# Kernel optimization log

Hardware: AMD Instinct MI355X
Metric: run time of the kernel (lower is better)

The kernel has to match this reference:

```python
import jax, jax.numpy as jnp
import numpy as np

N = 100000
E = 1600000
IN, HID, OUT = 128, 128, 64


def sage_conv(x, edge_index, W_l, W_r, b):
    # PyG SAGEConv with mean aggregation:
    # out = mean_{j in N(i)} x_j @ W_l + x_i @ W_r + b
    src, dst = edge_index[0], edge_index[1]
    msgs = x[src]                                            # [E, D] gather
    summed = jax.ops.segment_sum(msgs, dst, num_segments=N)  # [N, D] scatter-add
    deg = jax.ops.segment_sum(jnp.ones((E,), x.dtype), dst, num_segments=N)
    mean = summed / jnp.maximum(deg, 1.0)[:, None]
    return mean @ W_l + x @ W_r + b


def setup_inputs() -> dict:
    key = jax.random.key(0)
    ks = jax.random.split(key, 8)
    x = jax.random.normal(ks[0], (N, IN), dtype=jnp.float32)
    edge_index = jax.random.randint(ks[1], (2, E), 0, N, dtype=jnp.int64)
    s1 = 1.0 / np.sqrt(IN)
    s2 = 1.0 / np.sqrt(HID)
    W1_l = jax.random.uniform(ks[2], (IN, HID), jnp.float32, -s1, s1)
    W1_r = jax.random.uniform(ks[3], (IN, HID), jnp.float32, -s1, s1)
    b1 = jnp.zeros((HID,), jnp.float32)
    W2_l = jax.random.uniform(ks[4], (HID, OUT), jnp.float32, -s2, s2)
    W2_r = jax.random.uniform(ks[5], (HID, OUT), jnp.float32, -s2, s2)
    b2 = jnp.zeros((OUT,), jnp.float32)
    return {"x": x, "edge_index": edge_index, "W1_l": W1_l, "W1_r": W1_r,
            "b1": b1, "W2_l": W2_l, "W2_r": W2_r, "b2": b2}


def reference(x, edge_index, W1_l, W1_r, b1, W2_l, W2_r, b2):
    h = sage_conv(x, edge_index, W1_l, W1_r, b1)
    h = jax.nn.relu(h)
    out = sage_conv(h, edge_index, W2_l, W2_r, b2)
    return out
```

## Files before the change

kernel.cpp:

```cpp
#include <hip/hip_runtime.h>

#define NN 100000
#define NE 1600000
#define KB 782
#define BSH 7
#define MAXB 4096
#define PBLK 200

#define OFF_CC    0
#define OFF_RST   1024
#define OFF_RDG   101120
#define OFF_STAGE 201216
#define OFF_XB    3404288
#define OFF_XF8   9810432
#define OFF_MEANB 13013504
#define OFF_HB    19419648
#define OFF_W1LP  25825792
#define OFF_W1RP  (25825792 + 8192)
#define OFF_W2LP  (25825792 + 16384)
#define OFF_W2RP  (25825792 + 20480)

typedef __bf16 bf16x8 __attribute__((ext_vector_type(8)));
typedef float f32x4 __attribute__((ext_vector_type(4)));
typedef float f32x2 __attribute__((ext_vector_type(2)));

static __device__ __forceinline__ ushort f2bf(float f) {
    unsigned u = __float_as_uint(f);
    return (ushort)((u + 0x7fffu + ((u >> 16) & 1u)) >> 16);
}
static __device__ __forceinline__ float bflo(unsigned u) { return __uint_as_float(u << 16); }
static __device__ __forceinline__ float bfhi(unsigned u) { return __uint_as_float(u & 0xffff0000u); }

__global__ void cvt_kernel(const float* __restrict__ x, ushort* __restrict__ xb,
                           unsigned* __restrict__ xf8) {
    int i = blockIdx.x * 256 + threadIdx.x;
    float4 v = ((const float4*)x)[i];
    uint2 o;
    o.x = (unsigned)f2bf(v.x) | ((unsigned)f2bf(v.y) << 16);
    o.y = (unsigned)f2bf(v.z) | ((unsigned)f2bf(v.w) << 16);
    ((uint2*)xb)[i] = o;
    int p8 = __builtin_amdgcn_cvt_pk_fp8_f32(v.x, v.y, 0, false);
    p8 = __builtin_amdgcn_cvt_pk_fp8_f32(v.z, v.w, p8, true);
    xf8[i] = (unsigned)p8;
}

__global__ void pack_kernel(const float* __restrict__ W1l, const float* __restrict__ W1r,
                            const float* __restrict__ W2l, const float* __restrict__ W2r,
                            ushort* __restrict__ w1lp, ushort* __restrict__ w1rp,
                            ushort* __restrict__ w2lp, ushort* __restrict__ w2rp) {
    int blk = blockIdx.x;
    const float* W;
    ushort* out;
    int N, frag0;
    if (blk < 8)       { W = W1l; out = w1lp; N = 128; frag0 = blk * 4; }
    else if (blk < 16) { W = W1r; out = w1rp; N = 128; frag0 = (blk - 8) * 4; }
    else if (blk < 20) { W = W2l; out = w2lp; N = 64;  frag0 = (blk - 16) * 4; }
    else               { W = W2r; out = w2rp; N = 64;  frag0 = (blk - 20) * 4; }
    int lane = threadIdx.x & 63;
    int frag = frag0 + (threadIdx.x >> 6);
    int NT = N >> 4;
    int ktile = frag / NT, ntile = frag - ktile * NT;
    int k = ktile * 32 + (lane >> 4) * 8;
    int n = ntile * 16 + (lane & 15);
    ushort tmp[8];
#pragma unroll
    for (int j = 0; j < 8; ++j) tmp[j] = f2bf(W[(k + j) * N + n]);
    uint4 o;
    o.x = (unsigned)tmp[0] | ((unsigned)tmp[1] << 16);
    o.y = (unsigned)tmp[2] | ((unsigned)tmp[3] << 16);
    o.z = (unsigned)tmp[4] | ((unsigned)tmp[5] << 16);
    o.w = (unsigned)tmp[6] | ((unsigned)tmp[7] << 16);
    *(uint4*)&out[(frag * 64 + lane) * 8] = o;
}

__global__ __launch_bounds__(1024) void cpart_kernel(const int* __restrict__ src,
                                                     const int* __restrict__ dst,
                                                     int* __restrict__ cc,
                                                     unsigned* __restrict__ stage) {
    __shared__ int hist[KB];
    __shared__ int cur[KB];
    int t = threadIdx.x;
    int e0 = blockIdx.x * (NE / PBLK);
    int e1 = e0 + (NE / PBLK);
    for (int i = t; i < KB; i += 1024) hist[i] = 0;
    __syncthreads();
    for (int e = e0 + t; e < e1; e += 1024)
        atomicAdd(&hist[dst[e] >> BSH], 1);
    __syncthreads();
    for (int i = t; i < KB; i += 1024) {
        int c = hist[i];
        cur[i] = c ? atomicAdd(&cc[i], c) : 0;
    }
    __syncthreads();
    for (int e = e0 + t; e < e1; e += 1024) {
        int d = dst[e];
        int bkt = d >> BSH;
        int p = atomicAdd(&cur[bkt], 1);
        if (p < MAXB)
            stage[bkt * MAXB + p] = ((unsigned)(d & 127) << 17) | (unsigned)src[e];
    }
}

__global__ __launch_bounds__(256) void sort_kernel(unsigned* __restrict__ stage,
                                                   const int* __restrict__ cc,
                                                   int* __restrict__ rstart,
                                                   int* __restrict__ rdeg) {
    __shared__ unsigned ssrc[MAXB];
    __shared__ int sc[128];
    __shared__ int loff[129];
    __shared__ int lcur[128];
    int t = threadIdx.x;
    int b = blockIdx.x;
    unsigned* st = stage + b * MAXB;
    int cnt = min(cc[b], MAXB);

    if (t < 128) lcur[t] = 0;
    __syncthreads();
    for (int i = t; i < cnt; i += 256) atomicAdd(&lcur[st[i] >> 17], 1);
    __syncthreads();
    if (t < 128) sc[t] = lcur[t];
    __syncthreads();
    for (int off = 1; off < 128; off <<= 1) {
        int v = (t < 128 && t >= off) ? sc[t - off] : 0;
        __syncthreads();
        if (t < 128) sc[t] += v;
        __syncthreads();
    }
    if (t < 128) {
        int excl = (t == 0) ? 0 : sc[t - 1];
        loff[t] = excl;
        lcur[t] = excl;
    }
    if (t == 127) loff[128] = sc[127];
    __syncthreads();
    for (int i = t; i < cnt; i += 256) {
        unsigned v = st[i];
        int p = atomicAdd(&lcur[v >> 17], 1);
        ssrc[p] = v & 0x1FFFFu;
    }
    __syncthreads();
    for (int i = t; i < cnt; i += 256) st[i] = ssrc[i];
    int node0 = b << BSH;
    if (t < 128 && node0 + t < NN) {
        rstart[node0 + t] = b * MAXB + loff[t];
        rdeg[node0 + t] = loff[t + 1] - loff[t];
    }
}

__global__ __launch_bounds__(256) void agg1g_kernel(const unsigned* __restrict__ es,
                                                    const int* __restrict__ rstart,
                                                    const int* __restrict__ rdeg,
                                                    const unsigned* __restrict__ xf8,
                                                    ushort* __restrict__ meanb) {
    int t = threadIdx.x;
    int node = blockIdx.x * 16 + (t >> 4);
    int l4 = t & 15;
    int s0 = rstart[node];
    int deg = rdeg[node];
    const uint2* xv = (const uint2*)xf8;
    float a0 = 0.f, a1 = 0.f, a2 = 0.f, a3 = 0.f;
    float a4 = 0.f, a5 = 0.f, a6 = 0.f, a7 = 0.f;
    int e = 0;
    for (; e + 4 <= deg; e += 4) {
        int q0 = es[s0 + e + 0];
        int q1 = es[s0 + e + 1];
        int q2 = es[s0 + e + 2];
        int q3 = es[s0 + e + 3];
        uint2 u0 = xv[q0 * 16 + l4];
        uint2 u1 = xv[q1 * 16 + l4];
        uint2 u2 = xv[q2 * 16 + l4];
        uint2 u3 = xv[q3 * 16 + l4];
#pragma unroll
        for (int j = 0; j < 4; ++j) {
            unsigned lo = (j == 0) ? u0.x : (j == 1) ? u1.x : (j == 2) ? u2.x : u3.x;
            unsigned hi = (j == 0) ? u0.y : (j == 1) ? u1.y : (j == 2) ? u2.y : u3.y;
            f32x2 p0 = __builtin_amdgcn_cvt_pk_f32_fp8(lo, false);
            f32x2 p1 = __builtin_amdgcn_cvt_pk_f32_fp8(lo, true);
            f32x2 p2 = __builtin_amdgcn_cvt_pk_f32_fp8(hi, false);
            f32x2 p3 = __builtin_amdgcn_cvt_pk_f32_fp8(hi, true);
            a0 += p0.x; a1 += p0.y; a2 += p1.x; a3 += p1.y;
            a4 += p2.x; a5 += p2.y; a6 += p3.x; a7 += p3.y;
        }
    }
    for (; e < deg; ++e) {
        uint2 u = xv[es[s0 + e] * 16 + l4];
        f32x2 p0 = __builtin_amdgcn_cvt_pk_f32_fp8(u.x, false);
        f32x2 p1 = __builtin_amdgcn_cvt_pk_f32_fp8(u.x, true);
        f32x2 p2 = __builtin_amdgcn_cvt_pk_f32_fp8(u.y, false);
        f32x2 p3 = __builtin_amdgcn_cvt_pk_f32_fp8(u.y, true);
        a0 += p0.x; a1 += p0.y; a2 += p1.x; a3 += p1.y;
        a4 += p2.x; a5 += p2.y; a6 += p3.x; a7 += p3.y;
    }
    float inv = 1.0f / fmaxf((float)deg, 1.0f);
    uint4 o;
    o.x = (unsigned)f2bf(a0 * inv) | ((unsigned)f2bf(a1 * inv) << 16);
    o.y = (unsigned)f2bf(a2 * inv) | ((unsigned)f2bf(a3 * inv) << 16);
    o.z = (unsigned)f2bf(a4 * inv) | ((unsigned)f2bf(a5 * inv) << 16);
    o.w = (unsigned)f2bf(a6 * inv) | ((unsigned)f2bf(a7 * inv) << 16);
    *(uint4*)&meanb[node * 128 + 8 * l4] = o;
}

__global__ __launch_bounds__(256) void agg2g_kernel(const unsigned* __restrict__ es,
                                                    const int* __restrict__ rstart,
                                                    const int* __restrict__ rdeg,
                                                    const ushort* __restrict__ pb,
                                                    float* __restrict__ meanp) {
    int t = threadIdx.x;
    int node = blockIdx.x * 8 + (t >> 5);
    int l5 = t & 31;
    int s0 = rstart[node];
    int deg = rdeg[node];
    const unsigned* pbu = (const unsigned*)pb;
    float a0 = 0.f, a1 = 0.f;
    int e = 0;
    for (; e + 4 <= deg; e += 4) {
        unsigned u0 = pbu[es[s0 + e + 0] * 32 + l5];
        unsigned u1 = pbu[es[s0 + e + 1] * 32 + l5];
        unsigned u2 = pbu[es[s0 + e + 2] * 32 + l5];
        unsigned u3 = pbu[es[s0 + e + 3] * 32 + l5];
        a0 += bflo(u0) + bflo(u1) + bflo(u2) + bflo(u3);
        a1 += bfhi(u0) + bfhi(u1) + bfhi(u2) + bfhi(u3);
    }
    for (; e < deg; ++e) {
        unsigned u = pbu[es[s0 + e] * 32 + l5];
        a0 += bflo(u); a1 += bfhi(u);
    }
    float inv = 1.0f / fmaxf((float)deg, 1.0f);
    float2 o = {a0 * inv, a1 * inv};
    *(float2*)&meanp[node * 64 + 2 * l5] = o;
}

__global__ __launch_bounds__(256) void gemm1_kernel(const ushort* __restrict__ meanb,
                                                    const ushort* __restrict__ xb,
                                                    const ushort* __restrict__ w1lp,
                                                    const ushort* __restrict__ w1rp,
                                                    const float* __restrict__ b1,
                                                    const ushort* __restrict__ w2lp,
                                                    ushort* __restrict__ hb,
                                                    ushort* __restrict__ pb) {
    __shared__ ushort As[64 * 136];
    int t = threadIdx.x;
    int node0 = blockIdx.x * 64;
    int w = t >> 6, l = t & 63;
    int lrow = w * 16 + (l & 15);
    int lkq = (l >> 4) * 8;
    int cq = l & 15, rq = (l >> 4) * 4;

    f32x4 acc[8];
#pragma unroll
    for (int i = 0; i < 8; ++i) acc[i] = (f32x4){0.f, 0.f, 0.f, 0.f};

    {
        const uint4* g = (const uint4*)(meanb + (size_t)node0 * 128);
#pragma unroll
        for (int i = 0; i < 4; ++i) {
            int chunk = t + 256 * i;
            *(uint4*)&As[(chunk >> 4) * 136 + (chunk & 15) * 8] = g[chunk];
        }
    }
    __syncthreads();
#pragma unroll
    for (int kt = 0; kt < 4; ++kt) {
        bf16x8 a = *(const bf16x8*)&As[lrow * 136 + kt * 32 + lkq];
        const bf16x8* bp = (const bf16x8*)w1lp + (kt * 8) * 64 + l;
#pragma unroll
        for (int nt = 0; nt < 8; ++nt)
            acc[nt] = __builtin_amdgcn_mfma_f32_16x16x32_bf16(a, bp[nt * 64], acc[nt], 0, 0, 0);
    }
    __syncthreads();

    {
        const uint4* g = (const uint4*)(xb + (size_t)node0 * 128);
#pragma unroll
        for (int i = 0; i < 4; ++i) {
            int chunk = t + 256 * i;
            *(uint4*)&As[(chunk >> 4) * 136 + (chunk & 15) * 8] = g[chunk];
        }
    }
    __syncthreads();
#pragma unroll
    for (int kt = 0; kt < 4; ++kt) {
        bf16x8 a = *(const bf16x8*)&As[lrow * 136 + kt * 32 + lkq];
        const bf16x8* bp = (const bf16x8*)w1rp + (kt * 8) * 64 + l;
#pragma unroll
        for (int nt = 0; nt < 8; ++nt)
            acc[nt] = __builtin_amdgcn_mfma_f32_16x16x32_bf16(a, bp[nt * 64], acc[nt], 0, 0, 0);
    }
    __syncthreads();

#pragma unroll
    for (int nt = 0; nt < 8; ++nt) {
        int n = nt * 16 + cq;
        float bias = b1[n];
#pragma unroll
        for (int r = 0; r < 4; ++r) {
            float hv = fmaxf(acc[nt][r] + bias, 0.0f);
            As[(w * 16 + rq + r) * 136 + n] = f2bf(hv);
        }
    }
    __syncthreads();

    {
        uint4* g = (uint4*)(hb + (size_t)node0 * 128);
#pragma unroll
        for (int i = 0; i < 4; ++i) {
            int chunk = t + 256 * i;
            if (node0 + (chunk >> 4) < NN)
                g[chunk] = *(const uint4*)&As[(chunk >> 4) * 136 + (chunk & 15) * 8];
        }
    }

    f32x4 acc2[4];
#pragma unroll
    for (int i = 0; i < 4; ++i) acc2[i] = (f32x4){0.f, 0.f, 0.f, 0.f};
#pragma unroll
    for (int kt = 0; kt < 4; ++kt) {
        bf16x8 a = *(const bf16x8*)&As[lrow * 136 + kt * 32 + lkq];
        const bf16x8* bp = (const bf16x8*)w2lp + (kt * 4) * 64 + l;
#pragma unroll
        for (int nt = 0; nt < 4; ++nt)
            acc2[nt] = __builtin_amdgcn_mfma_f32_16x16x32_bf16(a, bp[nt * 64], acc2[nt], 0, 0, 0);
    }
    __syncthreads();

#pragma unroll
    for (int nt = 0; nt < 4; ++nt)
#pragma unroll
        for (int r = 0; r < 4; ++r)
            As[(w * 16 + rq + r) * 136 + nt * 16 + cq] = f2bf(acc2[nt][r]);
    __syncthreads();
    {
        uint4* g = (uint4*)(pb + (size_t)node0 * 64);
#pragma unroll
        for (int i = 0; i < 2; ++i) {
            int chunk = t + 256 * i;
            if (node0 + (chunk >> 3) < NN)
                g[chunk] = *(const uint4*)&As[(chunk >> 3) * 136 + (chunk & 7) * 8];
        }
    }
}

__global__ __launch_bounds__(256) void gemm2_kernel(const float* __restrict__ meanp,
                                                    const ushort* __restrict__ hb,
                                                    const ushort* __restrict__ w2rp,
                                                    const float* __restrict__ b2,
                                                    float* __restrict__ out) {
    __shared__ ushort As[64 * 136];
    int t = threadIdx.x;
    int node0 = blockIdx.x * 64;
    int w = t >> 6, l = t & 63;
    int lrow = w * 16 + (l & 15);
    int lkq = (l >> 4) * 8;
    int cq = l & 15, rq = (l >> 4) * 4;

    {
        const uint4* g = (const uint4*)(hb + (size_t)node0 * 128);
#pragma unroll
        for (int i = 0; i < 4; ++i) {
            int chunk = t + 256 * i;
            *(uint4*)&As[(chunk >> 4) * 136 + (chunk & 15) * 8] = g[chunk];
        }
    }
    __syncthreads();

    f32x4 acc[4];
#pragma unroll
    for (int i = 0; i < 4; ++i) acc[i] = (f32x4){0.f, 0.f, 0.f, 0.f};
#pragma unroll
    for (int kt = 0; kt < 4; ++kt) {
        bf16x8 a = *(const bf16x8*)&As[lrow * 136 + kt * 32 + lkq];
        const bf16x8* bp = (const bf16x8*)w2rp + (kt * 4) * 64 + l;
#pragma unroll
        for (int nt = 0; nt < 4; ++nt)
            acc[nt] = __builtin_amdgcn_mfma_f32_16x16x32_bf16(a, bp[nt * 64], acc[nt], 0, 0, 0);
    }

#pragma unroll
    for (int nt = 0; nt < 4; ++nt) {
        int n = nt * 16 + cq;
        float bias = b2[n];
#pragma unroll
        for (int r = 0; r < 4; ++r) {
            int row = node0 + w * 16 + rq + r;
            if (row < NN)
                out[(size_t)row * 64 + n] = acc[nt][r] + bias + meanp[(size_t)row * 64 + n];
        }
    }
}

extern "C" void kernel_launch(void* const* d_in, const int* in_sizes, int n_in,
                              void* d_out, int out_size, void* d_ws, size_t ws_size,
                              hipStream_t stream) {
    const float* x   = (const float*)d_in[0];
    const int*   ei  = (const int*)d_in[1];
    const float* W1l = (const float*)d_in[2];
    const float* W1r = (const float*)d_in[3];
    const float* b1  = (const float*)d_in[4];
    const float* W2l = (const float*)d_in[5];
    const float* W2r = (const float*)d_in[6];
    const float* b2  = (const float*)d_in[7];

    const int* src = ei;
    const int* dst = ei + NE;

    int*      ws_i   = (int*)d_ws;
    int*      cc     = ws_i + OFF_CC;
    int*      rstart = ws_i + OFF_RST;
    int*      rdeg   = ws_i + OFF_RDG;
    unsigned* stage  = (unsigned*)(ws_i + OFF_STAGE);
    ushort*   xb     = (ushort*)(ws_i + OFF_XB);
    unsigned* xf8    = (unsigned*)(ws_i + OFF_XF8);
    ushort*   pb     = (ushort*)(ws_i + OFF_XF8);
    ushort*   meanb  = (ushort*)(ws_i + OFF_MEANB);
    float*    meanp  = (float*)(ws_i + OFF_MEANB);
    ushort*   hb     = (ushort*)(ws_i + OFF_HB);
    ushort*   w1lp   = (ushort*)(ws_i + OFF_W1LP);
    ushort*   w1rp   = (ushort*)(ws_i + OFF_W1RP);
    ushort*   w2lp   = (ushort*)(ws_i + OFF_W2LP);
    ushort*   w2rp   = (ushort*)(ws_i + OFF_W2RP);

    hipMemsetAsync(cc, 0, 1024 * sizeof(int), stream);
    cvt_kernel<<<12500, 256, 0, stream>>>(x, xb, xf8);
    pack_kernel<<<24, 256, 0, stream>>>(W1l, W1r, W2l, W2r, w1lp, w1rp, w2lp, w2rp);
    cpart_kernel<<<PBLK, 1024, 0, stream>>>(src, dst, cc, stage);
    sort_kernel<<<KB, 256, 0, stream>>>(stage, cc, rstart, rdeg);

    agg1g_kernel<<<NN / 16, 256, 0, stream>>>(stage, rstart, rdeg, xf8, meanb);
    gemm1_kernel<<<(NN + 63) / 64, 256, 0, stream>>>(meanb, xb, w1lp, w1rp, b1, w2lp, hb, pb);

    agg2g_kernel<<<NN / 8, 256, 0, stream>>>(stage, rstart, rdeg, pb, meanp);
    gemm2_kernel<<<(NN + 63) / 64, 256, 0, stream>>>(meanp, hb, w2rp, b2, (float*)d_out);
}
```

Baseline: 271.0 us.

## Fuse neighbor-mean aggregation into both GEMM kernels via shared memory

The separate aggregation kernels for both layers are removed. Their gather-and-mean loops now run inside gemm1 and gemm2, and the means go straight into shared memory instead of a global intermediate buffer. This drops two kernel launches and the global write and re-read of the mean tensors. In exchange, each GEMM block does irregular gather work before its MFMA phase, so gather latency can no longer be hidden by a separate high-occupancy kernel. The per-block workload becomes imbalanced, and gemm2 uses more shared memory.

```diff
diff --git a/kernel.cpp b/kernel.cpp
--- a/kernel.cpp
+++ b/kernel.cpp
@@ -13,7 +13,7 @@
 #define OFF_STAGE 201216
 #define OFF_XB    3404288
 #define OFF_XF8   9810432
-#define OFF_MEANB 13013504
+#define OFF_PB    13013504
 #define OFF_HB    19419648
 #define OFF_W1LP  25825792
 #define OFF_W1RP  (25825792 + 8192)
@@ -147,90 +147,10 @@
     }
 }
 
-__global__ __launch_bounds__(256) void agg1g_kernel(const unsigned* __restrict__ es,
+__global__ __launch_bounds__(256) void gemm1_kernel(const unsigned* __restrict__ es,
                                                     const int* __restrict__ rstart,
                                                     const int* __restrict__ rdeg,
                                                     const unsigned* __restrict__ xf8,
-                                                    ushort* __restrict__ meanb) {
-    int t = threadIdx.x;
-    int node = blockIdx.x * 16 + (t >> 4);
-    int l4 = t & 15;
-    int s0 = rstart[node];
-    int deg = rdeg[node];
-    const uint2* xv = (const uint2*)xf8;
-    float a0 = 0.f, a1 = 0.f, a2 = 0.f, a3 = 0.f;
-    float a4 = 0.f, a5 = 0.f, a6 = 0.f, a7 = 0.f;
-    int e = 0;
-    for (; e + 4 <= deg; e += 4) {
-        int q0 = es[s0 + e + 0];
-        int q1 = es[s0 + e + 1];
-        int q2 = es[s0 + e + 2];
-        int q3 = es[s0 + e + 3];
-        uint2 u0 = xv[q0 * 16 + l4];
-        uint2 u1 = xv[q1 * 16 + l4];
-        uint2 u2 = xv[q2 * 16 + l4];
-        uint2 u3 = xv[q3 * 16 + l4];
-#pragma unroll
-        for (int j = 0; j < 4; ++j) {
-            unsigned lo = (j == 0) ? u0.x : (j == 1) ? u1.x : (j == 2) ? u2.x : u3.x;
-            unsigned hi = (j == 0) ? u0.y : (j == 1) ? u1.y : (j == 2) ? u2.y : u3.y;
-            f32x2 p0 = __builtin_amdgcn_cvt_pk_f32_fp8(lo, false);
-            f32x2 p1 = __builtin_amdgcn_cvt_pk_f32_fp8(lo, true);
-            f32x2 p2 = __builtin_amdgcn_cvt_pk_f32_fp8(hi, false);
-            f32x2 p3 = __builtin_amdgcn_cvt_pk_f32_fp8(hi, true);
-            a0 += p0.x; a1 += p0.y; a2 += p1.x; a3 += p1.y;
-            a4 += p2.x; a5 += p2.y; a6 += p3.x; a7 += p3.y;
-        }
-    }
-    for (; e < deg; ++e) {
-        uint2 u = xv[es[s0 + e] * 16 + l4];
-        f32x2 p0 = __builtin_amdgcn_cvt_pk_f32_fp8(u.x, false);
-        f32x2 p1 = __builtin_amdgcn_cvt_pk_f32_fp8(u.x, true);
-        f32x2 p2 = __builtin_amdgcn_cvt_pk_f32_fp8(u.y, false);
-        f32x2 p3 = __builtin_amdgcn_cvt_pk_f32_fp8(u.y, true);
-        a0 += p0.x; a1 += p0.y; a2 += p1.x; a3 += p1.y;
-        a4 += p2.x; a5 += p2.y; a6 += p3.x; a7 += p3.y;
-    }
-    float inv = 1.0f / fmaxf((float)deg, 1.0f);
-    uint4 o;
-    o.x = (unsigned)f2bf(a0 * inv) | ((unsigned)f2bf(a1 * inv) << 16);
-    o.y = (unsigned)f2bf(a2 * inv) | ((unsigned)f2bf(a3 * inv) << 16);
-    o.z = (unsigned)f2bf(a4 * inv) | ((unsigned)f2bf(a5 * inv) << 16);
-    o.w = (unsigned)f2bf(a6 * inv) | ((unsigned)f2bf(a7 * inv) << 16);
-    *(uint4*)&meanb[node * 128 + 8 * l4] = o;
-}
-
-__global__ __launch_bounds__(256) void agg2g_kernel(const unsigned* __restrict__ es,
-                                                    const int* __restrict__ rstart,
-                                                    const int* __restrict__ rdeg,
-                                                    const ushort* __restrict__ pb,
-                                                    float* __restrict__ meanp) {
-    int t = threadIdx.x;
-    int node = blockIdx.x * 8 + (t >> 5);
-    int l5 = t & 31;
-    int s0 = rstart[node];
-    int deg = rdeg[node];
-    const unsigned* pbu = (const unsigned*)pb;
-    float a0 = 0.f, a1 = 0.f;
-    int e = 0;
-    for (; e + 4 <= deg; e += 4) {
-        unsigned u0 = pbu[es[s0 + e + 0] * 32 + l5];
-        unsigned u1 = pbu[es[s0 + e + 1] * 32 + l5];
-        unsigned u2 = pbu[es[s0 + e + 2] * 32 + l5];
-        unsigned u3 = pbu[es[s0 + e + 3] * 32 + l5];
-        a0 += bflo(u0) + bflo(u1) + bflo(u2) + bflo(u3);
-        a1 += bfhi(u0) + bfhi(u1) + bfhi(u2) + bfhi(u3);
-    }
-    for (; e < deg; ++e) {
-        unsigned u = pbu[es[s0 + e] * 32 + l5];
-        a0 += bflo(u); a1 += bfhi(u);
-    }
-    float inv = 1.0f / fmaxf((float)deg, 1.0f);
-    float2 o = {a0 * inv, a1 * inv};
-    *(float2*)&meanp[node * 64 + 2 * l5] = o;
-}
-
-__global__ __launch_bounds__(256) void gemm1_kernel(const ushort* __restrict__ meanb,
                                                     const ushort* __restrict__ xb,
                                                     const ushort* __restrict__ w1lp,
                                                     const ushort* __restrict__ w1rp,
@@ -246,19 +166,66 @@
     int lkq = (l >> 4) * 8;
     int cq = l & 15, rq = (l >> 4) * 4;
 
+    {
+        int l4 = t & 15, grp = t >> 4;
+        const uint2* xv = (const uint2*)xf8;
+#pragma unroll
+        for (int i = 0; i < 4; ++i) {
+            int nl = i * 16 + grp;
+            int node = node0 + nl;
+            float a0 = 0.f, a1 = 0.f, a2 = 0.f, a3 = 0.f;
+            float a4 = 0.f, a5 = 0.f, a6 = 0.f, a7 = 0.f;
+            float inv = 0.f;
+            if (node < NN) {
+                int s0 = rstart[node];
+                int deg = rdeg[node];
+                int e = 0;
+                for (; e + 4 <= deg; e += 4) {
+                    int q0 = es[s0 + e + 0];
+                    int q1 = es[s0 + e + 1];
+                    int q2 = es[s0 + e + 2];
+                    int q3 = es[s0 + e + 3];
+                    uint2 u0 = xv[q0 * 16 + l4];
+                    uint2 u1 = xv[q1 * 16 + l4];
+                    uint2 u2 = xv[q2 * 16 + l4];
+                    uint2 u3 = xv[q3 * 16 + l4];
+#pragma unroll
+                    for (int j = 0; j < 4; ++j) {
+                        unsigned lo = (j == 0) ? u0.x : (j == 1) ? u1.x : (j == 2) ? u2.x : u3.x;
+                        unsigned hi = (j == 0) ? u0.y : (j == 1) ? u1.y : (j == 2) ? u2.y : u3.y;
+                        f32x2 p0 = __builtin_amdgcn_cvt_pk_f32_fp8(lo, false);
+                        f32x2 p1 = __builtin_amdgcn_cvt_pk_f32_fp8(lo, true);
+                        f32x2 p2 = __builtin_amdgcn_cvt_pk_f32_fp8(hi, false);
+                        f32x2 p3 = __builtin_amdgcn_cvt_pk_f32_fp8(hi, true);
+                        a0 += p0.x; a1 += p0.y; a2 += p1.x; a3 += p1.y;
+                        a4 += p2.x; a5 += p2.y; a6 += p3.x; a7 += p3.y;
+                    }
+                }
+                for (; e < deg; ++e) {
+                    uint2 u = xv[es[s0 + e] * 16 + l4];
+                    f32x2 p0 = __builtin_amdgcn_cvt_pk_f32_fp8(u.x, false);
+                    f32x2 p1 = __builtin_amdgcn_cvt_pk_f32_fp8(u.x, true);
+                    f32x2 p2 = __builtin_amdgcn_cvt_pk_f32_fp8(u.y, false);
+                    f32x2 p3 = __builtin_amdgcn_cvt_pk_f32_fp8(u.y, true);
+                    a0 += p0.x; a1 += p0.y; a2 += p1.x; a3 += p1.y;
+                    a4 += p2.x; a5 += p2.y; a6 += p3.x; a7 += p3.y;
+                }
+                inv = 1.0f / fmaxf((float)deg, 1.0f);
+            }
+            uint4 o;
+            o.x = (unsigned)f2bf(a0 * inv) | ((unsigned)f2bf(a1 * inv) << 16);
+            o.y = (unsigned)f2bf(a2 * inv) | ((unsigned)f2bf(a3 * inv) << 16);
+            o.z = (unsigned)f2bf(a4 * inv) | ((unsigned)f2bf(a5 * inv) << 16);
+            o.w = (unsigned)f2bf(a6 * inv) | ((unsigned)f2bf(a7 * inv) << 16);
+            *(uint4*)&As[nl * 136 + 8 * l4] = o;
+        }
+    }
+    __syncthreads();
+
     f32x4 acc[8];
 #pragma unroll
     for (int i = 0; i < 8; ++i) acc[i] = (f32x4){0.f, 0.f, 0.f, 0.f};
 
-    {
-        const uint4* g = (const uint4*)(meanb + (size_t)node0 * 128);
-#pragma unroll
-        for (int i = 0; i < 4; ++i) {
-            int chunk = t + 256 * i;
-            *(uint4*)&As[(chunk >> 4) * 136 + (chunk & 15) * 8] = g[chunk];
-        }
-    }
-    __syncthreads();
 #pragma unroll
     for (int kt = 0; kt < 4; ++kt) {
         bf16x8 a = *(const bf16x8*)&As[lrow * 136 + kt * 32 + lkq];
@@ -340,12 +307,16 @@
     }
 }
 
-__global__ __launch_bounds__(256) void gemm2_kernel(const float* __restrict__ meanp,
+__global__ __launch_bounds__(256) void gemm2_kernel(const unsigned* __restrict__ es,
+                                                    const int* __restrict__ rstart,
+                                                    const int* __restrict__ rdeg,
+                                                    const ushort* __restrict__ pbt,
                                                     const ushort* __restrict__ hb,
                                                     const ushort* __restrict__ w2rp,
                                                     const float* __restrict__ b2,
                                                     float* __restrict__ out) {
     __shared__ ushort As[64 * 136];
+    __shared__ unsigned ms[64 * 32];
     int t = threadIdx.x;
     int node0 = blockIdx.x * 64;
     int w = t >> 6, l = t & 63;
@@ -354,6 +325,37 @@
     int cq = l & 15, rq = (l >> 4) * 4;
 
     {
+        int l5 = t & 31, hw = t >> 5;
+        const unsigned* pbu = (const unsigned*)pbt;
+#pragma unroll
+        for (int i = 0; i < 8; ++i) {
+            int nl = i * 8 + hw;
+            int node = node0 + nl;
+            float a0 = 0.f, a1 = 0.f;
+            float inv = 0.f;
+            if (node < NN) {
+                int s0 = rstart[node];
+                int deg = rdeg[node];
+                int e = 0;
+                for (; e + 4 <= deg; e += 4) {
+                    unsigned u0 = pbu[es[s0 + e + 0] * 32 + l5];
+                    unsigned u1 = pbu[es[s0 + e + 1] * 32 + l5];
+                    unsigned u2 = pbu[es[s0 + e + 2] * 32 + l5];
+                    unsigned u3 = pbu[es[s0 + e + 3] * 32 + l5];
+                    a0 += bflo(u0) + bflo(u1) + bflo(u2) + bflo(u3);
+                    a1 += bfhi(u0) + bfhi(u1) + bfhi(u2) + bfhi(u3);
+                }
+                for (; e < deg; ++e) {
+                    unsigned u = pbu[es[s0 + e] * 32 + l5];
+                    a0 += bflo(u); a1 += bfhi(u);
+                }
+                inv = 1.0f / fmaxf((float)deg, 1.0f);
+            }
+            ms[nl * 32 + l5] = (unsigned)f2bf(a0 * inv) | ((unsigned)f2bf(a1 * inv) << 16);
+        }
+    }
+
+    {
         const uint4* g = (const uint4*)(hb + (size_t)node0 * 128);
 #pragma unroll
         for (int i = 0; i < 4; ++i) {
@@ -382,8 +384,11 @@
 #pragma unroll
         for (int r = 0; r < 4; ++r) {
             int row = node0 + w * 16 + rq + r;
-            if (row < NN)
-                out[(size_t)row * 64 + n] = acc[nt][r] + bias + meanp[(size_t)row * 64 + n];
+            if (row < NN) {
+                unsigned u = ms[(w * 16 + rq + r) * 32 + (n >> 1)];
+                float m = (n & 1) ? bfhi(u) : bflo(u);
+                out[(size_t)row * 64 + n] = acc[nt][r] + bias + m;
+            }
         }
     }
 }
@@ -410,9 +415,7 @@
     unsigned* stage  = (unsigned*)(ws_i + OFF_STAGE);
     ushort*   xb     = (ushort*)(ws_i + OFF_XB);
     unsigned* xf8    = (unsigned*)(ws_i + OFF_XF8);
-    ushort*   pb     = (ushort*)(ws_i + OFF_XF8);
-    ushort*   meanb  = (ushort*)(ws_i + OFF_MEANB);
-    float*    meanp  = (float*)(ws_i + OFF_MEANB);
+    ushort*   pb     = (ushort*)(ws_i + OFF_PB);
     ushort*   hb     = (ushort*)(ws_i + OFF_HB);
     ushort*   w1lp   = (ushort*)(ws_i + OFF_W1LP);
     ushort*   w1rp   = (ushort*)(ws_i + OFF_W1RP);
@@ -425,9 +428,9 @@
     cpart_kernel<<<PBLK, 1024, 0, stream>>>(src, dst, cc, stage);
     sort_kernel<<<KB, 256, 0, stream>>>(stage, cc, rstart, rdeg);
 
-    agg1g_kernel<<<NN / 16, 256, 0, stream>>>(stage, rstart, rdeg, xf8, meanb);
-    gemm1_kernel<<<(NN + 63) / 64, 256, 0, stream>>>(meanb, xb, w1lp, w1rp, b1, w2lp, hb, pb);
-
-    agg2g_kernel<<<NN / 8, 256, 0, stream>>>(stage, rstart, rdeg, pb, meanp);
-    gemm2_kernel<<<(NN + 63) / 64, 256, 0, stream>>>(meanp, hb, w2rp, b2, (float*)d_out);
-}
+    gemm1_kernel<<<(NN + 63) / 64, 256, 0, stream>>>(stage, rstart, rdeg, xf8, xb,
+                                                     w1lp, w1rp, b1, w2lp, hb, pb);
+
+    gemm2_kernel<<<(NN + 63) / 64, 256, 0, stream>>>(stage, rstart, rdeg, pb, hb,
+                                                     w2rp, b2, (float*)d_out);
+}
```

Result: slower. 298.1 us (+10.0%).
